# Optimization experiments

Hardware: AMD Instinct MI355X
Metric: run time of the kernel (lower is better)

Reference implementation:

```python
import jax, jax.numpy as jnp
import numpy as np

B, G, D, N_HEADS, FFN, L = 16, 2048, 256, 8, 1024, 4
HEAD_DIM = D // N_HEADS
EPS_LN = 1e-5
MASK_TOKEN = -10.0
REE_BASE = 100.0


def setup_inputs() -> dict:
    key = jax.random.key(0)
    ks = jax.random.split(key, 20)
    s = 0.02
    inp = {
        'x': jax.random.normal(ks[0], (B, G), jnp.float32),
        'gene_emb': jax.random.normal(ks[1], (G, D), jnp.float32) * s,
        'inv_freq': (1.0 / REE_BASE ** (jnp.arange(0, D, 2, dtype=jnp.float32) / D)),
        'Wq': jax.random.normal(ks[2], (L, D, D), jnp.float32) * s,
        'bq': jnp.zeros((L, D), jnp.float32),
        'Wk': jax.random.normal(ks[3], (L, D, D), jnp.float32) * s,
        'bk': jnp.zeros((L, D), jnp.float32),
        'Wv': jax.random.normal(ks[4], (L, D, D), jnp.float32) * s,
        'bv': jnp.zeros((L, D), jnp.float32),
        'ln1_g': jnp.ones((L, D), jnp.float32),
        'ln1_b': jnp.zeros((L, D), jnp.float32),
        'ln2_g': jnp.ones((L, D), jnp.float32),
        'ln2_b': jnp.zeros((L, D), jnp.float32),
        'WU': jax.random.normal(ks[5], (L, D, FFN), jnp.float32) * s,
        'bU': jnp.zeros((L, FFN), jnp.float32),
        'WV': jax.random.normal(ks[6], (L, FFN, D), jnp.float32) * s,
        'bV': jnp.zeros((L, D), jnp.float32),
        'Wout': jax.random.normal(ks[7], (D, 1), jnp.float32) * s,
        'bout': jnp.zeros((1,), jnp.float32),
    }
    return inp


def layernorm(x, g, b):
    m = x.mean(-1, keepdims=True)
    v = ((x - m) ** 2).mean(-1, keepdims=True)
    return (x - m) / jnp.sqrt(v + EPS_LN) * g + b


def causal_linear_attention(q, k, v):
    # q, k already feature-mapped ('sqr'); shapes [B, S, H, dh]
    b, s, h, dh = q.shape
    qs, ks_, vs = (jnp.moveaxis(t, 1, 0) for t in (q, k, v))  # [S,B,H,dh]
    num0 = jnp.zeros((b, h, dh, dh), q.dtype)
    den0 = jnp.zeros((b, h, dh), q.dtype)

    def step(carry, qkv):
        num_s, den_s = carry
        qt, kt, vt = qkv
        num_s = num_s + jnp.einsum('bhf,bhd->bhfd', kt, vt)
        den_s = den_s + kt
        num = jnp.einsum('bhf,bhfd->bhd', qt, num_s)
        den = jnp.einsum('bhf,bhf->bh', qt, den_s)
        return (num_s, den_s), num / (den[..., None] + 1e-16)

    _, out = jax.lax.scan(step, (num0, den0), (qs, ks_, vs))  # [S,B,H,dh]
    return jnp.moveaxis(out, 0, 1).reshape(b, s, h * dh)


def reference(x, gene_emb, inv_freq, Wq, bq, Wk, bk, Wv, bv,
              ln1_g, ln1_b, ln2_g, ln2_b, WU, bU, WV, bV, Wout, bout):
    b, g = x.shape
    # Rotary Expression Embedding
    freqs = x[..., None] * inv_freq  # [B,G,D/2]
    emb = jnp.concatenate([jnp.sin(freqs), jnp.cos(freqs)], axis=-1)  # [B,G,D]
    emb = jnp.where((x == MASK_TOKEN)[..., None], 0.0, emb)
    h = gene_emb[None] + emb  # [B,G,D]

    for l in range(Wq.shape[0]):
        hn = layernorm(h, ln1_g[l], ln1_b[l])  # pre-LN (on_gptln=True)
        q = (hn @ Wq[l] + bq[l]).reshape(b, g, N_HEADS, HEAD_DIM) ** 2
        k = (hn @ Wk[l] + bk[l]).reshape(b, g, N_HEADS, HEAD_DIM) ** 2
        v = (hn @ Wv[l] + bv[l]).reshape(b, g, N_HEADS, HEAD_DIM)
        h = h + causal_linear_attention(q, k, v)
        hn2 = layernorm(h, ln2_g[l], ln2_b[l])
        h = h + jax.nn.gelu(hn2 @ WU[l] + bU[l], approximate=False) @ WV[l] + bV[l]
    return (h @ Wout + bout).squeeze(-1)  # [B,G]
```

## Files before the change

kernel.cpp:

```cpp
#include <hip/hip_runtime.h>
#include <math.h>


#define GG 2048
#define DD 256
#define NROWS 32768
#define NC 32
#define CS 64

typedef __attribute__((ext_vector_type(8))) short bf16x8;
typedef __attribute__((ext_vector_type(4))) float f32x4;

struct FalseT { static constexpr bool value = false; };
struct TrueT  { static constexpr bool value = true;  };

__device__ __forceinline__ short f2bf(float f) {
  union { float f; unsigned u; } v; v.f = f;
  unsigned r = v.u + 0x7FFFu + ((v.u >> 16) & 1u);
  return (short)(r >> 16);
}
__device__ __forceinline__ float bf2f(short s) {
  union { unsigned u; float f; } v; v.u = ((unsigned)(unsigned short)s) << 16;
  return v.f;
}
__device__ __forceinline__ void gld16(const short* g, short* l) {
  __builtin_amdgcn_global_load_lds(
      (const __attribute__((address_space(1))) void*)g,
      (__attribute__((address_space(3))) void*)l, 16, 0, 0);
}
__device__ __forceinline__ float fast_gelu(float x) {
  float y = 1.595769122f * (x + 0.044715f * x * x * x);
  return x / (1.0f + __expf(-y));
}

__global__ __launch_bounds__(256) void embed_kernel(
    const float* __restrict__ x, const float* __restrict__ ge,
    const float* __restrict__ invf, float* __restrict__ h) {
  int bg = blockIdx.x * 4 + (threadIdx.x >> 6);
  int g = bg & (GG - 1);
  int lane = threadIdx.x & 63;
  float xv = x[bg];
  int d = lane * 4;
  float4 e;
  if (lane < 32) {
    float4 f = *(const float4*)&invf[d];
    e.x = sinf(xv * f.x); e.y = sinf(xv * f.y);
    e.z = sinf(xv * f.z); e.w = sinf(xv * f.w);
  } else {
    float4 f = *(const float4*)&invf[d - 128];
    e.x = cosf(xv * f.x); e.y = cosf(xv * f.y);
    e.z = cosf(xv * f.z); e.w = cosf(xv * f.w);
  }
  if (xv == -10.0f) { e.x = 0.f; e.y = 0.f; e.z = 0.f; e.w = 0.f; }
  float4 gv = *(const float4*)&ge[(size_t)g * DD + d];
  float4 o; o.x = gv.x + e.x; o.y = gv.y + e.y; o.z = gv.z + e.z; o.w = gv.w + e.w;
  *(float4*)&h[(size_t)bg * DD + d] = o;
}

__global__ __launch_bounds__(256) void ln_tiled(
    const float* __restrict__ h, const float* __restrict__ gamma,
    const float* __restrict__ beta, short* __restrict__ outT) {
  __shared__ float mean_s[32], rstd_s[32];
  __shared__ float gls[256], bls[256];
  int r0 = blockIdx.x * 32;
  int tid = threadIdx.x;
  gls[tid] = gamma[tid]; bls[tid] = beta[tid];
  {
    int row = tid >> 3, seg = tid & 7;
    const float4* hp = (const float4*)(h + (size_t)(r0 + row) * DD + seg * 32);
    float s = 0.f, s2 = 0.f;
#pragma unroll
    for (int i = 0; i < 8; ++i) {
      float4 v = hp[i];
      s += v.x + v.y + v.z + v.w;
      s2 += v.x * v.x + v.y * v.y + v.z * v.z + v.w * v.w;
    }
    s += __shfl_xor(s, 1); s += __shfl_xor(s, 2); s += __shfl_xor(s, 4);
    s2 += __shfl_xor(s2, 1); s2 += __shfl_xor(s2, 2); s2 += __shfl_xor(s2, 4);
    if (seg == 0) {
      float mn = s * (1.0f / 256.0f);
      mean_s[row] = mn;
      rstd_s[row] = rsqrtf(s2 * (1.0f / 256.0f) - mn * mn + 1e-5f);
    }
  }
  __syncthreads();
  int row = tid & 31, kc8 = (tid >> 5) & 3, half = tid >> 7;
  float mn = mean_s[row], rs = rstd_s[row];
  size_t hrow = (size_t)(r0 + row) * DD;
  int trow = (r0 & 127) + row;
  short* tb = outT + (size_t)(r0 >> 7) * 8 * 4096 + (kc8 * 128 + trow) * 8;
#pragma unroll
  for (int j = 0; j < 4; ++j) {
    int kb = half * 4 + j;
    int k0 = kb * 32 + kc8 * 8;
    float4 x0 = *(const float4*)&h[hrow + k0];
    float4 x1 = *(const float4*)&h[hrow + k0 + 4];
    float4 g0 = *(const float4*)&gls[k0], g1 = *(const float4*)&gls[k0 + 4];
    float4 b0 = *(const float4*)&bls[k0], b1 = *(const float4*)&bls[k0 + 4];
    bf16x8 aw;
    aw[0] = f2bf((x0.x - mn) * rs * g0.x + b0.x);
    aw[1] = f2bf((x0.y - mn) * rs * g0.y + b0.y);
    aw[2] = f2bf((x0.z - mn) * rs * g0.z + b0.z);
    aw[3] = f2bf((x0.w - mn) * rs * g0.w + b0.w);
    aw[4] = f2bf((x1.x - mn) * rs * g1.x + b1.x);
    aw[5] = f2bf((x1.y - mn) * rs * g1.y + b1.y);
    aw[6] = f2bf((x1.z - mn) * rs * g1.z + b1.z);
    aw[7] = f2bf((x1.w - mn) * rs * g1.w + b1.w);
    *(bf16x8*)&tb[(size_t)kb * 4096] = aw;
  }
}

__global__ __launch_bounds__(256) void prep_weights(
    const float* __restrict__ Wq, const float* __restrict__ Wk,
    const float* __restrict__ Wv, const float* __restrict__ WU,
    const float* __restrict__ WV,
    short* __restrict__ TQ, short* __restrict__ TK, short* __restrict__ TV,
    short* __restrict__ TU, short* __restrict__ TVd) {
  int zz = blockIdx.z, l = blockIdx.y;
  const float* src; short* dst; int Kd, Nd;
  if (zz == 0) { src = Wq; dst = TQ; Kd = 256; Nd = 256; }
  else if (zz == 1) { src = Wk; dst = TK; Kd = 256; Nd = 256; }
  else if (zz == 2) { src = Wv; dst = TV; Kd = 256; Nd = 256; }
  else if (zz == 3) { src = WU; dst = TU; Kd = 256; Nd = 1024; }
  else { src = WV; dst = TVd; Kd = 1024; Nd = 256; }
  int tot = Kd * Nd;
  int e = blockIdx.x * 256 + threadIdx.x;
  if (e >= tot) return;
  int t = e >> 12;
  int cslot = (e >> 3) & 511;
  int elem = e & 7;
  int kc8 = cslot >> 7, rn = cslot & 127;
  int nKb = Kd >> 5;
  int nt = t / nKb, kb = t - nt * nKb;
  int n = nt * 128 + rn, k = kb * 32 + kc8 * 8 + elem;
  dst[(size_t)l * tot + e] = f2bf(src[(size_t)l * tot + (size_t)k * Nd + n]);
}

template <int K, int EPI>
__global__ __launch_bounds__(256) void gemm_t(
    const short* __restrict__ A, const short* __restrict__ B0,
    const short* __restrict__ B1, const short* __restrict__ B2,
    const float* __restrict__ bias0, const float* __restrict__ bias1,
    const float* __restrict__ bias2,
    short* __restrict__ o0, short* __restrict__ o1, short* __restrict__ o2,
    float* __restrict__ outf, int N) {
  __shared__ __align__(16) short L[24576];
  constexpr int nIter = K / 32;
  int z = blockIdx.z;
  const short* Bt = (z == 0) ? B0 : (z == 1) ? B1 : B2;
  const float* bias = (z == 0) ? bias0 : (z == 1) ? bias1 : bias2;
  short* outz = (z == 0) ? o0 : (z == 1) ? o1 : o2;
  int m0 = blockIdx.x * 128, n0 = blockIdx.y * 128;
  int tid = threadIdx.x;
  int lane = tid & 63, w = tid >> 6;
  int q = lane >> 4, r = lane & 15;
  int wm = (w >> 1) * 64, wn = (w & 1) * 64;
  const short* At = A + (size_t)blockIdx.x * nIter * 4096;
  const short* Btl = Bt + (size_t)blockIdx.y * nIter * 4096;
  f32x4 vzero = {0.f, 0.f, 0.f, 0.f};
  f32x4 acc[4][4];
#pragma unroll
  for (int i = 0; i < 4; ++i)
#pragma unroll
    for (int j = 0; j < 4; ++j) acc[i][j] = vzero;

  int c0 = tid * 8, c1 = (tid + 256) * 8;
#pragma unroll
  for (int g = 0; g < 3; ++g) {
    gld16(At + g * 4096 + c0, &L[g * 4096 + c0]);
    gld16(At + g * 4096 + c1, &L[g * 4096 + c1]);
    gld16(Btl + g * 4096 + c0, &L[12288 + g * 4096 + c0]);
    gld16(Btl + g * 4096 + c1, &L[12288 + g * 4096 + c1]);
  }

  int abase = (q * 128 + wm + r) * 8;
  int bbase = (q * 128 + wn + r) * 8;

#pragma unroll
  for (int gi = 0; gi < nIter; ++gi) {
    const int rem = nIter - 1 - gi;
    if (rem >= 2)      __builtin_amdgcn_s_waitcnt(0x0f78);
    else if (rem == 1) __builtin_amdgcn_s_waitcnt(0x0f74);
    else               __builtin_amdgcn_s_waitcnt(0x0f70);
    __builtin_amdgcn_s_barrier();
    __builtin_amdgcn_s_setprio(1);
    const int cur = gi % 3;
    const short* Asc = &L[cur * 4096];
    const short* Bsc = &L[12288 + cur * 4096];
    bf16x8 af[4], bfr[4];
#pragma unroll
    for (int mt = 0; mt < 4; ++mt)
      af[mt] = *(const bf16x8*)&Asc[abase + mt * 16 * 8];
#pragma unroll
    for (int nt = 0; nt < 4; ++nt)
      bfr[nt] = *(const bf16x8*)&Bsc[bbase + nt * 16 * 8];
#pragma unroll
    for (int mt = 0; mt < 4; ++mt)
#pragma unroll
      for (int nt = 0; nt < 4; ++nt)
        acc[mt][nt] = __builtin_amdgcn_mfma_f32_16x16x32_bf16(bfr[nt], af[mt], acc[mt][nt], 0, 0, 0);
    __builtin_amdgcn_s_setprio(0);
    __builtin_amdgcn_s_waitcnt(0xc07f);
    __builtin_amdgcn_s_barrier();
    if (gi + 3 < nIter) {
      size_t kn = (size_t)(gi + 3) * 4096;
      gld16(At + kn + c0, &L[cur * 4096 + c0]);
      gld16(At + kn + c1, &L[cur * 4096 + c1]);
      gld16(Btl + kn + c0, &L[12288 + cur * 4096 + c0]);
      gld16(Btl + kn + c1, &L[12288 + cur * 4096 + c1]);
    }
  }

  float4 bias4[4];
#pragma unroll
  for (int nt = 0; nt < 4; ++nt) bias4[nt] = *(const float4*)&bias[n0 + wn + nt * 16 + q * 4];

  if (EPI == 0) {
    short* T = L;
#pragma unroll
    for (int mt = 0; mt < 4; ++mt) {
      int ml = wm + mt * 16 + r;
#pragma unroll
      for (int nt = 0; nt < 4; ++nt) {
        f32x4 v = acc[mt][nt];
        v[0] += bias4[nt].x; v[1] += bias4[nt].y; v[2] += bias4[nt].z; v[3] += bias4[nt].w;
        if (z < 2) { v[0] *= v[0]; v[1] *= v[1]; v[2] *= v[2]; v[3] *= v[3]; }
        short4 pk; pk.x = f2bf(v[0]); pk.y = f2bf(v[1]); pk.z = f2bf(v[2]); pk.w = f2bf(v[3]);
        *(short4*)&T[ml * 132 + wn + nt * 16 + q * 4] = pk;
      }
    }
    __syncthreads();
#pragma unroll
    for (int t2 = 0; t2 < 2; ++t2) {
      int task = tid + t2 * 256;
      int row = task & 127, hl = task >> 7;
      size_t obase = ((size_t)((n0 >> 5) + hl) * NROWS + m0 + row) * 32;
#pragma unroll
      for (int j = 0; j < 4; ++j)
        *(bf16x8*)&outz[obase + j * 8] = *(const bf16x8*)&T[row * 132 + hl * 32 + j * 8];
    }
  } else if (EPI == 1) {
#pragma unroll
    for (int mt = 0; mt < 4; ++mt) {
      int ml = wm + mt * 16 + r;
#pragma unroll
      for (int nt = 0; nt < 4; ++nt) {
        f32x4 v = acc[mt][nt];
        v[0] += bias4[nt].x; v[1] += bias4[nt].y; v[2] += bias4[nt].z; v[3] += bias4[nt].w;
#pragma unroll
        for (int e = 0; e < 4; ++e) v[e] = fast_gelu(v[e]);
        short4 o; o.x = f2bf(v[0]); o.y = f2bf(v[1]); o.z = f2bf(v[2]); o.w = f2bf(v[3]);
        int n = n0 + wn + nt * 16 + q * 4;
        size_t ti = ((size_t)blockIdx.x * (N >> 5) + (n >> 5)) * 4096 +
                    (size_t)(((n >> 3) & 3) << 10) + (ml << 3) + (n & 7);
        *(short4*)&outz[ti] = o;
      }
    }
  } else {
    float* TF = (float*)L;
#pragma unroll
    for (int half = 0; half < 2; ++half) {
      __syncthreads();
      if ((w & 1) == half) {
#pragma unroll
        for (int mt = 0; mt < 4; ++mt) {
          int ml = wm + mt * 16 + r;
#pragma unroll
          for (int nt = 0; nt < 4; ++nt) {
            f32x4 v = acc[mt][nt];
            v[0] += bias4[nt].x; v[1] += bias4[nt].y; v[2] += bias4[nt].z; v[3] += bias4[nt].w;
            *(f32x4*)&TF[ml * 68 + nt * 16 + q * 4] = v;
          }
        }
      }
      __syncthreads();
      int row = tid >> 1, col = (tid & 1) * 32;
      size_t hoff = (size_t)(m0 + row) * N + n0 + half * 64 + col;
#pragma unroll
      for (int j = 0; j < 8; ++j) {
        float4 add = *(const float4*)&TF[row * 68 + col + j * 4];
        float4 cur4 = *(float4*)&outf[hoff + j * 4];
        cur4.x += add.x; cur4.y += add.y; cur4.z += add.z; cur4.w += add.w;
        *(float4*)&outf[hoff + j * 4] = cur4;
      }
    }
  }
}

__global__ __launch_bounds__(512) void ffn_fused(
    const short* __restrict__ A, const short* __restrict__ TUw,
    const short* __restrict__ TVw, const float* __restrict__ bUp,
    const float* __restrict__ bVp, float* __restrict__ h,
    short* __restrict__ hnT, const float* __restrict__ ln1g,
    const float* __restrict__ ln1b) {
  __shared__ __align__(16) short L[81920];
  int tid = threadIdx.x;
  int lane = tid & 63, w = tid >> 6;
  int q = lane >> 4, r = lane & 15;
  int wmU = (w >> 2) * 64, wnU = (w & 3) * 32;
  int wmD = (w >> 2) * 64, wnD = (w & 3) * 64;
  const short* At = A + (size_t)blockIdx.x * 32768;

#pragma unroll
  for (int i = 0; i < 8; ++i)
    gld16(At + (i * 512 + tid) * 8, &L[(i * 512 + tid) * 8]);

  auto issueFor = [&](int t) {
    short* dst = &L[49152 + (t & 1) * 16384];
    int ss = t >> 2, pp = t & 3;
    if (pp < 2) {
      const short* g0 = TUw + ((size_t)ss * 8 + pp * 4) * 4096;
#pragma unroll
      for (int i = 0; i < 4; ++i)
        gld16(g0 + (i * 512 + tid) * 8, dst + (i * 512 + tid) * 8);
    } else {
      int kbg0 = ss * 4 + (pp - 2) * 2;
#pragma unroll
      for (int kl = 0; kl < 2; ++kl) {
        gld16(TVw + (size_t)(kbg0 + kl) * 4096 + tid * 8,
              dst + kl * 8192 + tid * 8);
        gld16(TVw + (size_t)(32 + kbg0 + kl) * 4096 + tid * 8,
              dst + kl * 8192 + 4096 + tid * 8);
      }
    }
  };

  issueFor(0); issueFor(1);

  f32x4 vzero = {0.f, 0.f, 0.f, 0.f};
  f32x4 accm[4][2], acco[4][4];
#pragma unroll
  for (int mt = 0; mt < 4; ++mt) {
#pragma unroll
    for (int nt = 0; nt < 2; ++nt) accm[mt][nt] = vzero;
#pragma unroll
    for (int nt = 0; nt < 4; ++nt) acco[mt][nt] = vzero;
  }
  float4 b4[2];

  auto slice = [&](int s, auto lastc) {
    constexpr bool LAST = decltype(lastc)::value;
#pragma unroll
    for (int p = 0; p < 2; ++p) {
      int sig = s * 4 + p;
      __builtin_amdgcn_s_waitcnt(0x0f74);
      __builtin_amdgcn_s_barrier();
      const short* Ws = &L[49152 + (sig & 1) * 16384];
#pragma unroll
      for (int kl = 0; kl < 4; ++kl) {
        int kb = p * 4 + kl;
        bf16x8 af[4], bfr[2];
#pragma unroll
        for (int mt = 0; mt < 4; ++mt)
          af[mt] = *(const bf16x8*)&L[kb * 4096 + (q * 128 + wmU + mt * 16 + r) * 8];
#pragma unroll
        for (int nt = 0; nt < 2; ++nt)
          bfr[nt] = *(const bf16x8*)&Ws[kl * 4096 + (q * 128 + wnU + nt * 16 + r) * 8];
#pragma unroll
        for (int mt = 0; mt < 4; ++mt)
#pragma unroll
          for (int nt = 0; nt < 2; ++nt)
            accm[mt][nt] = __builtin_amdgcn_mfma_f32_16x16x32_bf16(
                bfr[nt], af[mt], accm[mt][nt], 0, 0, 0);
      }
      if (p == 1) {
#pragma unroll
        for (int mt = 0; mt < 4; ++mt) {
          int row = wmU + mt * 16 + r;
#pragma unroll
          for (int nt = 0; nt < 2; ++nt) {
            f32x4 v = accm[mt][nt];
            float4 bb = b4[nt];
            v[0] += bb.x; v[1] += bb.y; v[2] += bb.z; v[3] += bb.w;
            short4 pk;
            pk.x = f2bf(fast_gelu(v[0])); pk.y = f2bf(fast_gelu(v[1]));
            pk.z = f2bf(fast_gelu(v[2])); pk.w = f2bf(fast_gelu(v[3]));
            int kc8 = 2 * nt + (q >> 1);
            *(short4*)&L[32768 + (w & 3) * 4096 + (kc8 * 128 + row) * 8 + (q & 1) * 4] = pk;
            accm[mt][nt] = vzero;
          }
        }
      }
      __builtin_amdgcn_s_waitcnt(0xc07f);
      __builtin_amdgcn_s_barrier();
      if (p == 0) {
        b4[0] = *(const float4*)&bUp[s * 128 + wnU + q * 4];
        b4[1] = *(const float4*)&bUp[s * 128 + wnU + 16 + q * 4];
      }
      if (sig + 2 < 32) issueFor(sig + 2);
    }
#pragma unroll
    for (int p2 = 0; p2 < 2; ++p2) {
      int sig = s * 4 + 2 + p2;
      if (LAST && p2 == 1) __builtin_amdgcn_s_waitcnt(0x0f70);
      else                 __builtin_amdgcn_s_waitcnt(0x0f74);
      __builtin_amdgcn_s_barrier();
      const short* Ws = &L[49152 + (sig & 1) * 16384];
#pragma unroll
      for (int kl = 0; kl < 2; ++kl) {
        int mtile = p2 * 2 + kl;
        bf16x8 am[4], bvf[4];
#pragma unroll
        for (int mt = 0; mt < 4; ++mt)
          am[mt] = *(const bf16x8*)&L[32768 + mtile * 4096 + (q * 128 + wmD + mt * 16 + r) * 8];
#pragma unroll
        for (int nt = 0; nt < 4; ++nt)
          bvf[nt] = *(const bf16x8*)&Ws[kl * 8192 + (wnD >> 7) * 4096 +
                                        (q * 128 + (wnD & 127) + nt * 16 + r) * 8];
#pragma unroll
        for (int mt = 0; mt < 4; ++mt)
#pragma unroll
          for (int nt = 0; nt < 4; ++nt)
            acco[mt][nt] = __builtin_amdgcn_mfma_f32_16x16x32_bf16(
                bvf[nt], am[mt], acco[mt][nt], 0, 0, 0);
      }
      __builtin_amdgcn_s_waitcnt(0xc07f);
      __builtin_amdgcn_s_barrier();
      if (sig + 2 < 32) issueFor(sig + 2);
    }
  };

  for (int s = 0; s < 7; ++s) slice(s, FalseT{});
  slice(7, TrueT{});

  float* TF = (float*)L;
  float* MEAN = (float*)&L[68608];
  float* RSTD = MEAN + 128;
  float4 bv4[4];
#pragma unroll
  for (int nt = 0; nt < 4; ++nt) bv4[nt] = *(const float4*)&bVp[wnD + nt * 16 + q * 4];
#pragma unroll
  for (int mt = 0; mt < 4; ++mt) {
    int row = wmD + mt * 16 + r;
#pragma unroll
    for (int nt = 0; nt < 4; ++nt) {
      f32x4 v = acco[mt][nt];
      v[0] += bv4[nt].x; v[1] += bv4[nt].y; v[2] += bv4[nt].z; v[3] += bv4[nt].w;
      *(f32x4*)&TF[row * 268 + wnD + nt * 16 + q * 4] = v;
    }
  }
  __syncthreads();
#pragma unroll
  for (int p = 0; p < 16; ++p) {
    int row = p * 8 + w;
    int col = lane * 4;
    size_t off = ((size_t)blockIdx.x * 128 + row) * DD + col;
    float4 ad = *(const float4*)&TF[row * 268 + col];
    float4 cv = *(float4*)&h[off];
    cv.x += ad.x; cv.y += ad.y; cv.z += ad.z; cv.w += ad.w;
    *(float4*)&h[off] = cv;
    if (ln1g) {
      *(float4*)&TF[row * 268 + col] = cv;
      float s = cv.x + cv.y + cv.z + cv.w;
      float s2 = cv.x * cv.x + cv.y * cv.y + cv.z * cv.z + cv.w * cv.w;
      s += __shfl_xor(s, 1); s += __shfl_xor(s, 2); s += __shfl_xor(s, 4);
      s += __shfl_xor(s, 8); s += __shfl_xor(s, 16); s += __shfl_xor(s, 32);
      s2 += __shfl_xor(s2, 1); s2 += __shfl_xor(s2, 2); s2 += __shfl_xor(s2, 4);
      s2 += __shfl_xor(s2, 8); s2 += __shfl_xor(s2, 16); s2 += __shfl_xor(s2, 32);
      if (lane == 0) {
        float mn = s * (1.0f / 256.0f);
        MEAN[row] = mn;
        RSTD[row] = rsqrtf(s2 * (1.0f / 256.0f) - mn * mn + 1e-5f);
      }
    }
  }
  if (ln1g) {
    __syncthreads();
    int row2 = tid & 127, kc8g = tid >> 7;
    float mn = MEAN[row2], rstd = RSTD[row2];
    short* tb = hnT + (size_t)blockIdx.x * 32768 + (kc8g * 128 + row2) * 8;
#pragma unroll
    for (int kb = 0; kb < 8; ++kb) {
      int k0 = kb * 32 + kc8g * 8;
      float4 x0 = *(const float4*)&TF[row2 * 268 + k0];
      float4 x1 = *(const float4*)&TF[row2 * 268 + k0 + 4];
      float4 g0 = *(const float4*)&ln1g[k0], g1 = *(const float4*)&ln1g[k0 + 4];
      float4 b0 = *(const float4*)&ln1b[k0], b1 = *(const float4*)&ln1b[k0 + 4];
      bf16x8 aw;
      aw[0] = f2bf((x0.x - mn) * rstd * g0.x + b0.x);
      aw[1] = f2bf((x0.y - mn) * rstd * g0.y + b0.y);
      aw[2] = f2bf((x0.z - mn) * rstd * g0.z + b0.z);
      aw[3] = f2bf((x0.w - mn) * rstd * g0.w + b0.w);
      aw[4] = f2bf((x1.x - mn) * rstd * g1.x + b1.x);
      aw[5] = f2bf((x1.y - mn) * rstd * g1.y + b1.y);
      aw[6] = f2bf((x1.z - mn) * rstd * g1.z + b1.z);
      aw[7] = f2bf((x1.w - mn) * rstd * g1.w + b1.w);
      *(bf16x8*)&tb[(size_t)kb * 4096] = aw;
    }
  }
}

__global__ __launch_bounds__(256) void attn_chunk_kv(
    const short* __restrict__ Kb, const short* __restrict__ Vb,
    float* __restrict__ St, float* __restrict__ Zc) {
  __shared__ short Kt[4][32 * 72];
  __shared__ short Vt[4][32 * 72];
  int wid = threadIdx.x >> 6;
  int blk = blockIdx.x * 4 + wid;
  int c = blk & (NC - 1), bh = blk >> 5;
  int b = bh >> 3, hh = bh & 7;
  int lane = threadIdx.x & 63, q = lane >> 4, r = lane & 15;
  size_t rowbase = ((size_t)hh * NROWS + b * GG + c * CS + lane) * 32;
#pragma unroll
  for (int j = 0; j < 4; ++j) {
    bf16x8 kv = *(const bf16x8*)&Kb[rowbase + j * 8];
    bf16x8 vv = *(const bf16x8*)&Vb[rowbase + j * 8];
#pragma unroll
    for (int e = 0; e < 8; ++e) {
      Kt[wid][(j * 8 + e) * 72 + lane] = kv[e];
      Vt[wid][(j * 8 + e) * 72 + lane] = vv[e];
    }
  }
  __syncthreads();
  f32x4 vzero = {0.f, 0.f, 0.f, 0.f};
  f32x4 acc[2][2];
#pragma unroll
  for (int i = 0; i < 2; ++i)
#pragma unroll
    for (int j = 0; j < 2; ++j) acc[i][j] = vzero;
#pragma unroll
  for (int ks = 0; ks < 2; ++ks) {
    bf16x8 afr[2], bfr[2];
#pragma unroll
    for (int mt = 0; mt < 2; ++mt) afr[mt] = *(const bf16x8*)&Kt[wid][(mt * 16 + r) * 72 + ks * 32 + q * 8];
#pragma unroll
    for (int nt = 0; nt < 2; ++nt) bfr[nt] = *(const bf16x8*)&Vt[wid][(nt * 16 + r) * 72 + ks * 32 + q * 8];
#pragma unroll
    for (int mt = 0; mt < 2; ++mt)
#pragma unroll
      for (int nt = 0; nt < 2; ++nt)
        acc[mt][nt] = __builtin_amdgcn_mfma_f32_16x16x32_bf16(afr[mt], bfr[nt], acc[mt][nt], 0, 0, 0);
  }
  float* stp = St + ((size_t)bh * NC + c) * 1024;
#pragma unroll
  for (int mt = 0; mt < 2; ++mt)
#pragma unroll
    for (int nt = 0; nt < 2; ++nt)
      *(f32x4*)&stp[(nt * 16 + r) * 32 + mt * 16 + q * 4] = acc[mt][nt];
  if (lane < 32) {
    float s = 0.f;
#pragma unroll
    for (int j = 0; j < 8; ++j) {
      bf16x8 kr = *(const bf16x8*)&Kt[wid][lane * 72 + j * 8];
#pragma unroll
      for (int e = 0; e < 8; ++e) s += bf2f(kr[e]);
    }
    Zc[((size_t)bh * NC + c) * 32 + lane] = s;
  }
}

__global__ __launch_bounds__(1024) void attn_prefix(float* __restrict__ St, float* __restrict__ Zc) {
  int bh = blockIdx.x, i = threadIdx.x;
  float run = 0.f;
  float* p = St + (size_t)bh * NC * 1024 + i;
#pragma unroll
  for (int c = 0; c < NC; ++c) { float t = p[(size_t)c * 1024]; p[(size_t)c * 1024] = run; run += t; }
  if (i < 32) {
    float rz = 0.f;
    float* pz = Zc + (size_t)bh * NC * 32 + i;
#pragma unroll
    for (int c = 0; c < NC; ++c) { float t = pz[c * 32]; pz[c * 32] = rz; rz += t; }
  }
}

__global__ __launch_bounds__(512) void attn_intra(
    const short* __restrict__ Qb, const short* __restrict__ Kb,
    const short* __restrict__ Vb, const float* __restrict__ St,
    const float* __restrict__ Zc, float* __restrict__ h,
    short* __restrict__ hnT, const float* __restrict__ ln2g,
    const float* __restrict__ ln2b) {
  __shared__ __align__(16) short P[8][64 * 72];
  __shared__ short Vt[8][32 * 72];
  __shared__ float den[8][64];
  __shared__ float MEAN[64], RSTD[64];
  int wid = threadIdx.x >> 6;
  int u = blockIdx.x;
  int b = u >> 5, c = u & 31;
  int hh = wid, bh = b * 8 + hh;
  int lane = threadIdx.x & 63, q = lane >> 4, r = lane & 15;
  size_t hrow0 = (size_t)b * GG + c * CS;
  size_t qrow0 = (size_t)hh * NROWS + b * GG + c * CS;

  const float* zp = Zc + ((size_t)bh * NC + c) * 32;
  float qz = 0.f;
  {
    size_t qoff = (qrow0 + lane) * 32;
#pragma unroll
    for (int j = 0; j < 4; ++j) {
      bf16x8 qv = *(const bf16x8*)&Qb[qoff + j * 8];
#pragma unroll
      for (int e = 0; e < 8; ++e) qz += bf2f(qv[e]) * zp[j * 8 + e];
    }
  }
  den[wid][lane] = qz;

  {
    size_t voff = (qrow0 + lane) * 32;
#pragma unroll
    for (int j = 0; j < 4; ++j) {
      bf16x8 vv = *(const bf16x8*)&Vb[voff + j * 8];
#pragma unroll
      for (int e = 0; e < 8; ++e) Vt[wid][(j * 8 + e) * 72 + lane] = vv[e];
    }
  }

  bf16x8 ak[4], bqf[4];
#pragma unroll
  for (int t4 = 0; t4 < 4; ++t4) {
    ak[t4]  = *(const bf16x8*)&Kb[(qrow0 + t4 * 16 + r) * 32 + q * 8];
    bqf[t4] = *(const bf16x8*)&Qb[(qrow0 + t4 * 16 + r) * 32 + q * 8];
  }
  f32x4 vzero = {0.f, 0.f, 0.f, 0.f};
  f32x4 pacc[4][4];
#pragma unroll
  for (int mt = 0; mt < 4; ++mt)
#pragma unroll
    for (int nt = 0; nt < 4; ++nt)
      pacc[mt][nt] = __builtin_amdgcn_mfma_f32_16x16x32_bf16(ak[mt], bqf[nt], vzero, 0, 0, 0);

  float rs[4] = {0.f, 0.f, 0.f, 0.f};
#pragma unroll
  for (int nt = 0; nt < 4; ++nt) {
    int t = nt * 16 + r;
#pragma unroll
    for (int mt = 0; mt < 4; ++mt) {
      short4 pk;
#pragma unroll
      for (int rr = 0; rr < 4; ++rr) {
        int s = mt * 16 + q * 4 + rr;
        float pv = (s <= t) ? pacc[mt][nt][rr] : 0.f;
        rs[nt] += pv;
        ((short*)&pk)[rr] = f2bf(pv);
      }
      *(short4*)&P[wid][t * 72 + mt * 16 + q * 4] = pk;
    }
  }
#pragma unroll
  for (int nt = 0; nt < 4; ++nt) {
    rs[nt] += __shfl_xor(rs[nt], 16);
    rs[nt] += __shfl_xor(rs[nt], 32);
  }
  __syncthreads();
  if (lane < 16) {
#pragma unroll
    for (int nt = 0; nt < 4; ++nt) den[wid][nt * 16 + lane] += rs[nt];
  }
  __syncthreads();

  f32x4 oacc[4][2];
#pragma unroll
  for (int mt = 0; mt < 4; ++mt)
#pragma unroll
    for (int nt2 = 0; nt2 < 2; ++nt2) oacc[mt][nt2] = vzero;
  const float* stp = St + ((size_t)bh * NC + c) * 1024;
#pragma unroll
  for (int nt2 = 0; nt2 < 2; ++nt2) {
    float4 s0 = *(const float4*)&stp[(nt2 * 16 + r) * 32 + q * 8];
    float4 s1 = *(const float4*)&stp[(nt2 * 16 + r) * 32 + q * 8 + 4];
    bf16x8 bs;
    bs[0] = f2bf(s0.x); bs[1] = f2bf(s0.y); bs[2] = f2bf(s0.z); bs[3] = f2bf(s0.w);
    bs[4] = f2bf(s1.x); bs[5] = f2bf(s1.y); bs[6] = f2bf(s1.z); bs[7] = f2bf(s1.w);
#pragma unroll
    for (int mt = 0; mt < 4; ++mt)
      oacc[mt][nt2] = __builtin_amdgcn_mfma_f32_16x16x32_bf16(bqf[mt], bs, oacc[mt][nt2], 0, 0, 0);
  }
#pragma unroll
  for (int ks = 0; ks < 2; ++ks) {
    bf16x8 ap[4];
#pragma unroll
    for (int mt = 0; mt < 4; ++mt)
      ap[mt] = *(const bf16x8*)&P[wid][(mt * 16 + r) * 72 + ks * 32 + q * 8];
#pragma unroll
    for (int nt2 = 0; nt2 < 2; ++nt2) {
      bf16x8 bv_ = *(const bf16x8*)&Vt[wid][(nt2 * 16 + r) * 72 + ks * 32 + q * 8];
#pragma unroll
      for (int mt = 0; mt < 4; ++mt)
        oacc[mt][nt2] = __builtin_amdgcn_mfma_f32_16x16x32_bf16(ap[mt], bv_, oacc[mt][nt2], 0, 0, 0);
    }
  }

  float* OF = (float*)&P[0][0];
  __syncthreads();
#pragma unroll
  for (int mt = 0; mt < 4; ++mt) {
#pragma unroll
    for (int rr = 0; rr < 4; ++rr) {
      int t = mt * 16 + q * 4 + rr;
      float inv = 1.0f / (den[wid][t] + 1e-16f);
#pragma unroll
      for (int nt2 = 0; nt2 < 2; ++nt2)
        OF[t * 268 + hh * 32 + nt2 * 16 + r] = oacc[mt][nt2][rr] * inv;
    }
  }
  __syncthreads();
  int tid = threadIdx.x;
#pragma unroll
  for (int p = 0; p < 8; ++p) {
    int row = p * 8 + wid;
    int col = lane * 4;
    size_t off = (hrow0 + row) * DD + col;
    float4 ad = *(const float4*)&OF[row * 268 + col];
    float4 cv = *(float4*)&h[off];
    cv.x += ad.x; cv.y += ad.y; cv.z += ad.z; cv.w += ad.w;
    *(float4*)&h[off] = cv;
    *(float4*)&OF[row * 268 + col] = cv;
    float s = cv.x + cv.y + cv.z + cv.w;
    float s2 = cv.x * cv.x + cv.y * cv.y + cv.z * cv.z + cv.w * cv.w;
    s += __shfl_xor(s, 1); s += __shfl_xor(s, 2); s += __shfl_xor(s, 4);
    s += __shfl_xor(s, 8); s += __shfl_xor(s, 16); s += __shfl_xor(s, 32);
    s2 += __shfl_xor(s2, 1); s2 += __shfl_xor(s2, 2); s2 += __shfl_xor(s2, 4);
    s2 += __shfl_xor(s2, 8); s2 += __shfl_xor(s2, 16); s2 += __shfl_xor(s2, 32);
    if (lane == 0) {
      float mn = s * (1.0f / 256.0f);
      MEAN[row] = mn;
      RSTD[row] = rsqrtf(s2 * (1.0f / 256.0f) - mn * mn + 1e-5f);
    }
  }
  __syncthreads();
  int row2 = tid & 63, kc8g = (tid >> 6) & 3, half = tid >> 8;
  float mn = MEAN[row2], rstd = RSTD[row2];
  size_t grow = hrow0 + row2;
  short* tb = hnT + (grow >> 7) * 32768 + (kc8g * 128 + (int)(grow & 127)) * 8;
#pragma unroll
  for (int j = 0; j < 4; ++j) {
    int kb = half * 4 + j;
    int k0 = kb * 32 + kc8g * 8;
    float4 x0 = *(const float4*)&OF[row2 * 268 + k0];
    float4 x1 = *(const float4*)&OF[row2 * 268 + k0 + 4];
    float4 g0 = *(const float4*)&ln2g[k0], g1 = *(const float4*)&ln2g[k0 + 4];
    float4 b0 = *(const float4*)&ln2b[k0], b1 = *(const float4*)&ln2b[k0 + 4];
    bf16x8 aw;
    aw[0] = f2bf((x0.x - mn) * rstd * g0.x + b0.x);
    aw[1] = f2bf((x0.y - mn) * rstd * g0.y + b0.y);
    aw[2] = f2bf((x0.z - mn) * rstd * g0.z + b0.z);
    aw[3] = f2bf((x0.w - mn) * rstd * g0.w + b0.w);
    aw[4] = f2bf((x1.x - mn) * rstd * g1.x + b1.x);
    aw[5] = f2bf((x1.y - mn) * rstd * g1.y + b1.y);
    aw[6] = f2bf((x1.z - mn) * rstd * g1.z + b1.z);
    aw[7] = f2bf((x1.w - mn) * rstd * g1.w + b1.w);
    *(bf16x8*)&tb[(size_t)kb * 4096] = aw;
  }
}

__global__ __launch_bounds__(256) void out_proj(
    const float* __restrict__ h, const float* __restrict__ Wout,
    const float* __restrict__ bout, float* __restrict__ out) {
  int row = blockIdx.x * 4 + (threadIdx.x >> 6);
  int lane = threadIdx.x & 63;
  float4 a = *(const float4*)&h[(size_t)row * DD + lane * 4];
  float4 w = *(const float4*)&Wout[lane * 4];
  float s = a.x * w.x + a.y * w.y + a.z * w.z + a.w * w.w;
#pragma unroll
  for (int o = 1; o < 64; o <<= 1) s += __shfl_xor(s, o);
  if (lane == 0) out[row] = s + bout[0];
}

extern "C" void kernel_launch(void* const* d_in, const int* in_sizes, int n_in,
                              void* d_out, int out_size, void* d_ws, size_t ws_size,
                              hipStream_t stream) {
  const float* x    = (const float*)d_in[0];
  const float* ge   = (const float*)d_in[1];
  const float* invf = (const float*)d_in[2];
  const float* Wq   = (const float*)d_in[3];
  const float* bq   = (const float*)d_in[4];
  const float* Wk   = (const float*)d_in[5];
  const float* bk   = (const float*)d_in[6];
  const float* Wv   = (const float*)d_in[7];
  const float* bv   = (const float*)d_in[8];
  const float* ln1g = (const float*)d_in[9];
  const float* ln1b = (const float*)d_in[10];
  const float* ln2g = (const float*)d_in[11];
  const float* ln2b = (const float*)d_in[12];
  const float* WU   = (const float*)d_in[13];
  const float* bU   = (const float*)d_in[14];
  const float* WV   = (const float*)d_in[15];
  const float* bV   = (const float*)d_in[16];
  const float* Wout = (const float*)d_in[17];
  const float* bout = (const float*)d_in[18];
  float* out = (float*)d_out;

  char* ws = (char*)d_ws;
  float* h   = (float*)(ws + 0);
  short* hn  = (short*)(ws + 33554432);
  char*  R   = ws + 50331648;
  short* qb  = (short*)(R + 0);
  short* kb  = (short*)(R + 16777216);
  short* vb  = (short*)(R + 33554432);
  float* St  = (float*)(R + 50331648);
  float* Zc  = (float*)(R + 67108864);
  char*  WT  = R + 67633152;
  short* TQ  = (short*)(WT + 0);
  short* TK  = (short*)(WT + 524288);
  short* TVq = (short*)(WT + 1048576);
  short* TU  = (short*)(WT + 1572864);
  short* TVd = (short*)(WT + 3670016);

  prep_weights<<<dim3(1024, 4, 5), 256, 0, stream>>>(Wq, Wk, Wv, WU, WV, TQ, TK, TVq, TU, TVd);
  embed_kernel<<<NROWS / 4, 256, 0, stream>>>(x, ge, invf, h);
  ln_tiled<<<NROWS / 32, 256, 0, stream>>>(h, ln1g, ln1b, hn);

  for (int l = 0; l < 4; ++l) {
    gemm_t<256, 0><<<dim3(256, 2, 3), 256, 0, stream>>>(
        hn, TQ + l * 65536, TK + l * 65536, TVq + l * 65536,
        bq + l * 256, bk + l * 256, bv + l * 256,
        qb, kb, vb, nullptr, 256);
    attn_chunk_kv<<<1024, 256, 0, stream>>>(kb, vb, St, Zc);
    attn_prefix<<<128, 1024, 0, stream>>>(St, Zc);
    attn_intra<<<512, 512, 0, stream>>>(qb, kb, vb, St, Zc, h,
                                        hn, ln2g + l * 256, ln2b + l * 256);
    ffn_fused<<<256, 512, 0, stream>>>(hn, TU + l * 262144, TVd + l * 262144,
                                       bU + l * 1024, bV + l * 256, h,
                                       hn,
                                       (l < 3) ? ln1g + (l + 1) * 256 : nullptr,
                                       (l < 3) ? ln1b + (l + 1) * 256 : nullptr);
  }
  out_proj<<<NROWS / 4, 256, 0, stream>>>(h, Wout, bout, out);
}
```

Baseline: 710.1 us.

## Fuse embed+LN, fold prefix scan into chunk kernel, fuse output projection

Result: slower. 1.424 ms (+100.5%).

```diff
diff --git a/kernel.cpp b/kernel.cpp
--- a/kernel.cpp
+++ b/kernel.cpp
@@ -33,9 +33,11 @@
   return x / (1.0f + __expf(-y));
 }
 
-__global__ __launch_bounds__(256) void embed_kernel(
+__global__ __launch_bounds__(256) void embed_ln(
     const float* __restrict__ x, const float* __restrict__ ge,
-    const float* __restrict__ invf, float* __restrict__ h) {
+    const float* __restrict__ invf, const float* __restrict__ gamma,
+    const float* __restrict__ beta, float* __restrict__ h,
+    short* __restrict__ hnT) {
   int bg = blockIdx.x * 4 + (threadIdx.x >> 6);
   int g = bg & (GG - 1);
   int lane = threadIdx.x & 63;
@@ -55,59 +57,24 @@
   float4 gv = *(const float4*)&ge[(size_t)g * DD + d];
   float4 o; o.x = gv.x + e.x; o.y = gv.y + e.y; o.z = gv.z + e.z; o.w = gv.w + e.w;
   *(float4*)&h[(size_t)bg * DD + d] = o;
-}
-
-__global__ __launch_bounds__(256) void ln_tiled(
-    const float* __restrict__ h, const float* __restrict__ gamma,
-    const float* __restrict__ beta, short* __restrict__ outT) {
-  __shared__ float mean_s[32], rstd_s[32];
-  __shared__ float gls[256], bls[256];
-  int r0 = blockIdx.x * 32;
-  int tid = threadIdx.x;
-  gls[tid] = gamma[tid]; bls[tid] = beta[tid];
-  {
-    int row = tid >> 3, seg = tid & 7;
-    const float4* hp = (const float4*)(h + (size_t)(r0 + row) * DD + seg * 32);
-    float s = 0.f, s2 = 0.f;
-#pragma unroll
-    for (int i = 0; i < 8; ++i) {
-      float4 v = hp[i];
-      s += v.x + v.y + v.z + v.w;
-      s2 += v.x * v.x + v.y * v.y + v.z * v.z + v.w * v.w;
-    }
-    s += __shfl_xor(s, 1); s += __shfl_xor(s, 2); s += __shfl_xor(s, 4);
-    s2 += __shfl_xor(s2, 1); s2 += __shfl_xor(s2, 2); s2 += __shfl_xor(s2, 4);
-    if (seg == 0) {
-      float mn = s * (1.0f / 256.0f);
-      mean_s[row] = mn;
-      rstd_s[row] = rsqrtf(s2 * (1.0f / 256.0f) - mn * mn + 1e-5f);
-    }
-  }
-  __syncthreads();
-  int row = tid & 31, kc8 = (tid >> 5) & 3, half = tid >> 7;
-  float mn = mean_s[row], rs = rstd_s[row];
-  size_t hrow = (size_t)(r0 + row) * DD;
-  int trow = (r0 & 127) + row;
-  short* tb = outT + (size_t)(r0 >> 7) * 8 * 4096 + (kc8 * 128 + trow) * 8;
-#pragma unroll
-  for (int j = 0; j < 4; ++j) {
-    int kb = half * 4 + j;
-    int k0 = kb * 32 + kc8 * 8;
-    float4 x0 = *(const float4*)&h[hrow + k0];
-    float4 x1 = *(const float4*)&h[hrow + k0 + 4];
-    float4 g0 = *(const float4*)&gls[k0], g1 = *(const float4*)&gls[k0 + 4];
-    float4 b0 = *(const float4*)&bls[k0], b1 = *(const float4*)&bls[k0 + 4];
-    bf16x8 aw;
-    aw[0] = f2bf((x0.x - mn) * rs * g0.x + b0.x);
-    aw[1] = f2bf((x0.y - mn) * rs * g0.y + b0.y);
-    aw[2] = f2bf((x0.z - mn) * rs * g0.z + b0.z);
-    aw[3] = f2bf((x0.w - mn) * rs * g0.w + b0.w);
-    aw[4] = f2bf((x1.x - mn) * rs * g1.x + b1.x);
-    aw[5] = f2bf((x1.y - mn) * rs * g1.y + b1.y);
-    aw[6] = f2bf((x1.z - mn) * rs * g1.z + b1.z);
-    aw[7] = f2bf((x1.w - mn) * rs * g1.w + b1.w);
-    *(bf16x8*)&tb[(size_t)kb * 4096] = aw;
-  }
+  float s = o.x + o.y + o.z + o.w;
+  float s2 = o.x * o.x + o.y * o.y + o.z * o.z + o.w * o.w;
+  s += __shfl_xor(s, 1); s += __shfl_xor(s, 2); s += __shfl_xor(s, 4);
+  s += __shfl_xor(s, 8); s += __shfl_xor(s, 16); s += __shfl_xor(s, 32);
+  s2 += __shfl_xor(s2, 1); s2 += __shfl_xor(s2, 2); s2 += __shfl_xor(s2, 4);
+  s2 += __shfl_xor(s2, 8); s2 += __shfl_xor(s2, 16); s2 += __shfl_xor(s2, 32);
+  float mn = s * (1.0f / 256.0f);
+  float rstd = rsqrtf(s2 * (1.0f / 256.0f) - mn * mn + 1e-5f);
+  float4 gm = *(const float4*)&gamma[d];
+  float4 bt = *(const float4*)&beta[d];
+  short4 pk;
+  pk.x = f2bf((o.x - mn) * rstd * gm.x + bt.x);
+  pk.y = f2bf((o.y - mn) * rstd * gm.y + bt.y);
+  pk.z = f2bf((o.z - mn) * rstd * gm.z + bt.z);
+  pk.w = f2bf((o.w - mn) * rstd * gm.w + bt.w);
+  short* tb = hnT + (size_t)(bg >> 7) * 32768 + (size_t)(d >> 5) * 4096 +
+              ((((d >> 3) & 3) * 128) + (bg & 127)) * 8 + (d & 7);
+  *(short4*)tb = pk;
 }
 
 __global__ __launch_bounds__(256) void prep_weights(
@@ -292,7 +259,8 @@
     const short* __restrict__ TVw, const float* __restrict__ bUp,
     const float* __restrict__ bVp, float* __restrict__ h,
     short* __restrict__ hnT, const float* __restrict__ ln1g,
-    const float* __restrict__ ln1b) {
+    const float* __restrict__ ln1b, const float* __restrict__ Woutp,
+    const float* __restrict__ boutp, float* __restrict__ outp) {
   __shared__ __align__(16) short L[81920];
   int tid = threadIdx.x;
   int lane = tid & 63, w = tid >> 6;
@@ -440,6 +408,7 @@
     }
   }
   __syncthreads();
+  float bo = outp ? boutp[0] : 0.f;
 #pragma unroll
   for (int p = 0; p < 16; ++p) {
     int row = p * 8 + w;
@@ -463,6 +432,13 @@
         RSTD[row] = rsqrtf(s2 * (1.0f / 256.0f) - mn * mn + 1e-5f);
       }
     }
+    if (outp) {
+      float4 w4 = *(const float4*)&Woutp[col];
+      float so = cv.x * w4.x + cv.y * w4.y + cv.z * w4.z + cv.w * w4.w;
+      so += __shfl_xor(so, 1); so += __shfl_xor(so, 2); so += __shfl_xor(so, 4);
+      so += __shfl_xor(so, 8); so += __shfl_xor(so, 16); so += __shfl_xor(so, 32);
+      if (lane == 0) outp[(size_t)blockIdx.x * 128 + row] = so + bo;
+    }
   }
   if (ln1g) {
     __syncthreads();
@@ -492,9 +468,10 @@
 
 __global__ __launch_bounds__(256) void attn_chunk_kv(
     const short* __restrict__ Kb, const short* __restrict__ Vb,
-    float* __restrict__ St, float* __restrict__ Zc) {
+    float* __restrict__ St, float* __restrict__ Zc, int* __restrict__ cnt) {
   __shared__ short Kt[4][32 * 72];
   __shared__ short Vt[4][32 * 72];
+  __shared__ int sflag;
   int wid = threadIdx.x >> 6;
   int blk = blockIdx.x * 4 + wid;
   int c = blk & (NC - 1), bh = blk >> 5;
@@ -547,19 +524,32 @@
     }
     Zc[((size_t)bh * NC + c) * 32 + lane] = s;
   }
-}
-
-__global__ __launch_bounds__(1024) void attn_prefix(float* __restrict__ St, float* __restrict__ Zc) {
-  int bh = blockIdx.x, i = threadIdx.x;
-  float run = 0.f;
-  float* p = St + (size_t)bh * NC * 1024 + i;
-#pragma unroll
-  for (int c = 0; c < NC; ++c) { float t = p[(size_t)c * 1024]; p[(size_t)c * 1024] = run; run += t; }
-  if (i < 32) {
-    float rz = 0.f;
-    float* pz = Zc + (size_t)bh * NC * 32 + i;
-#pragma unroll
-    for (int c = 0; c < NC; ++c) { float t = pz[c * 32]; pz[c * 32] = rz; rz += t; }
+
+  __threadfence();
+  __syncthreads();
+  if (threadIdx.x == 0) sflag = (atomicAdd(&cnt[bh], 4) == 28);
+  __syncthreads();
+  if (!sflag) return;
+  __threadfence();
+  {
+    int t = threadIdx.x;
+    float* p = St + (size_t)bh * NC * 1024;
+    float* p0 = p + t, *p1 = p + t + 256, *p2 = p + t + 512, *p3 = p + t + 768;
+    float r0 = 0.f, r1 = 0.f, r2 = 0.f, r3 = 0.f;
+#pragma unroll
+    for (int c2 = 0; c2 < NC; ++c2) {
+      float v0 = p0[c2 * 1024], v1 = p1[c2 * 1024];
+      float v2 = p2[c2 * 1024], v3 = p3[c2 * 1024];
+      p0[c2 * 1024] = r0; p1[c2 * 1024] = r1;
+      p2[c2 * 1024] = r2; p3[c2 * 1024] = r3;
+      r0 += v0; r1 += v1; r2 += v2; r3 += v3;
+    }
+    if (t < 32) {
+      float rz = 0.f;
+      float* pz = Zc + (size_t)bh * NC * 32 + t;
+#pragma unroll
+      for (int c2 = 0; c2 < NC; ++c2) { float v = pz[c2 * 32]; pz[c2 * 32] = rz; rz += v; }
+    }
   }
 }
 
@@ -740,19 +730,6 @@
     aw[7] = f2bf((x1.w - mn) * rstd * g1.w + b1.w);
     *(bf16x8*)&tb[(size_t)kb * 4096] = aw;
   }
-}
-
-__global__ __launch_bounds__(256) void out_proj(
-    const float* __restrict__ h, const float* __restrict__ Wout,
-    const float* __restrict__ bout, float* __restrict__ out) {
-  int row = blockIdx.x * 4 + (threadIdx.x >> 6);
-  int lane = threadIdx.x & 63;
-  float4 a = *(const float4*)&h[(size_t)row * DD + lane * 4];
-  float4 w = *(const float4*)&Wout[lane * 4];
-  float s = a.x * w.x + a.y * w.y + a.z * w.z + a.w * w.w;
-#pragma unroll
-  for (int o = 1; o < 64; o <<= 1) s += __shfl_xor(s, o);
-  if (lane == 0) out[row] = s + bout[0];
 }
 
 extern "C" void kernel_launch(void* const* d_in, const int* in_sizes, int n_in,
@@ -794,25 +771,27 @@
   short* TVq = (short*)(WT + 1048576);
   short* TU  = (short*)(WT + 1572864);
   short* TVd = (short*)(WT + 3670016);
-
+  int*   cnt = (int*)(WT + 5767168);
+
+  hipMemsetAsync(cnt, 0, 4 * 128 * sizeof(int), stream);
   prep_weights<<<dim3(1024, 4, 5), 256, 0, stream>>>(Wq, Wk, Wv, WU, WV, TQ, TK, TVq, TU, TVd);
-  embed_kernel<<<NROWS / 4, 256, 0, stream>>>(x, ge, invf, h);
-  ln_tiled<<<NROWS / 32, 256, 0, stream>>>(h, ln1g, ln1b, hn);
+  embed_ln<<<NROWS / 4, 256, 0, stream>>>(x, ge, invf, ln1g, ln1b, h, hn);
 
   for (int l = 0; l < 4; ++l) {
     gemm_t<256, 0><<<dim3(256, 2, 3), 256, 0, stream>>>(
         hn, TQ + l * 65536, TK + l * 65536, TVq + l * 65536,
         bq + l * 256, bk + l * 256, bv + l * 256,
         qb, kb, vb, nullptr, 256);
-    attn_chunk_kv<<<1024, 256, 0, stream>>>(kb, vb, St, Zc);
-    attn_prefix<<<128, 1024, 0, stream>>>(St, Zc);
+    attn_chunk_kv<<<1024, 256, 0, stream>>>(kb, vb, St, Zc, cnt + l * 128);
     attn_intra<<<512, 512, 0, stream>>>(qb, kb, vb, St, Zc, h,
                                         hn, ln2g + l * 256, ln2b + l * 256);
     ffn_fused<<<256, 512, 0, stream>>>(hn, TU + l * 262144, TVd + l * 262144,
                                        bU + l * 1024, bV + l * 256, h,
                                        hn,
                                        (l < 3) ? ln1g + (l + 1) * 256 : nullptr,
-                                       (l < 3) ? ln1b + (l + 1) * 256 : nullptr);
-  }
-  out_proj<<<NROWS / 4, 256, 0, stream>>>(h, Wout, bout, out);
-}
+                                       (l < 3) ? ln1b + (l + 1) * 256 : nullptr,
+                                       (l == 3) ? Wout : nullptr,
+                                       (l == 3) ? bout : nullptr,
+                                       (l == 3) ? out : nullptr);
+  }
+}
```
